# Kernel tuning notes

Hardware: AMD Instinct MI355X
Metric: run time of the kernel (lower is better)

Reference implementation:

```python
import jax, jax.numpy as jnp
import numpy as np

N_NODES = 50000


def gcn_conv(x, W, b, src, dst, n_nodes):
    """PyG GCNConv: h = x @ W; symmetric-normalized aggregation with self-loops; + bias."""
    h = x @ W  # [N, F_out]
    ones = jnp.ones(src.shape[0], dtype=h.dtype)
    # degree including the self-loop (edge weight 1)
    deg = jax.ops.segment_sum(ones, dst, num_segments=n_nodes) + 1.0
    dinv = jax.lax.rsqrt(deg)  # deg >= 1, always valid
    norm = dinv[src] * dinv[dst]  # [E]
    msgs = h[src] * norm[:, None]  # [E, F_out]
    agg = jax.ops.segment_sum(msgs, dst, num_segments=n_nodes)
    agg = agg + h * (dinv * dinv)[:, None]  # self-loop contribution, norm = dinv_i^2
    return agg + b


def setup_inputs() -> dict:
    key = jax.random.key(0)
    ks = jax.random.split(key, 8)
    n, f_in, f_hid, f_out, n_edges = N_NODES, 128, 128, 40, 800000
    x = jax.random.normal(ks[0], (n, f_in), dtype=jnp.float32)
    edge_index = jax.random.randint(ks[1], (2, n_edges), 0, n, dtype=jnp.int64)
    new_edge_indexs = jax.random.randint(ks[2], (2, 1000), 0, n, dtype=jnp.int64)
    # Glorot init like PyG defaults
    s1 = (6.0 / (f_in + f_hid)) ** 0.5
    s2 = (6.0 / (f_hid + f_out)) ** 0.5
    W1 = jax.random.uniform(ks[3], (f_in, f_hid), jnp.float32, -s1, s1)
    b1 = jnp.zeros((f_hid,), jnp.float32)
    W2 = jax.random.uniform(ks[4], (f_hid, f_out), jnp.float32, -s2, s2)
    b2 = jnp.zeros((f_out,), jnp.float32)
    return {"x": x, "W1": W1, "b1": b1, "W2": W2, "b2": b2,
            "edge_index": edge_index, "new_edge_indexs": new_edge_indexs}


def reference(x, W1, b1, W2, b2, edge_index, new_edge_indexs):
    src, dst = edge_index[0], edge_index[1]
    h = gcn_conv(x, W1, b1, src, dst, N_NODES)
    h = jax.nn.relu(h)
    # dropout(p=0.5) is identity in eval mode (training=False)
    h = gcn_conv(h, W2, b2, src, dst, N_NODES)
    return jax.nn.log_softmax(h, axis=-1)
```

## Files before the change

kernel.cpp:

```cpp
#include <hip/hip_runtime.h>
#include <hip/hip_bf16.h>

#define N_NODES 50000
#define N_EDGES 800000
#define F_IN    128
#define F_HID   128
#define F_OUT   40
#define N_TILES (N_NODES / 16)

#define NBIN      98
#define BIN_SHIFT 9
#define EPB       1024
#define CAP       32
#define GBIN_CAP  9216

#define CVT_BLOCKS ((F_IN * F_HID + 48 * F_HID) / 256)
#define DEGZ_BLOCKS 196
#define BIN_BLOCKS ((N_EDGES + EPB - 1) / EPB)
#define G1_BLOCKS  ((N_TILES + 3) / 4)

typedef __attribute__((ext_vector_type(8))) short bf16x8;
typedef __attribute__((ext_vector_type(4))) float f32x4;

__device__ __forceinline__ float2 unpack_bf2(unsigned u) {
    float2 r;
    r.x = __uint_as_float(u << 16);
    r.y = __uint_as_float(u & 0xffff0000u);
    return r;
}
__device__ __forceinline__ unsigned pack_bf2(float x, float y) {
    union { unsigned u; __hip_bfloat16 h[2]; } cv;
    cv.h[0] = __float2bfloat16(x);
    cv.h[1] = __float2bfloat16(y);
    return cv.u;
}
__device__ __forceinline__ short bfraw(float v) {
    __hip_bfloat16 h = __float2bfloat16(v);
    return *(short*)&h;
}
__device__ __forceinline__ float bf16u_to_f32(unsigned short us) {
    return __uint_as_float(((unsigned)us) << 16);
}

__device__ __forceinline__ int ld_src(const unsigned int* w, int is64, int e) {
    return is64 ? (int)w[2 * e] : (int)w[e];
}
__device__ __forceinline__ int ld_dst(const unsigned int* w, int is64, int e) {
    return is64 ? (int)w[2 * (N_EDGES + e)] : (int)w[N_EDGES + e];
}

__global__ void k_init(const unsigned int* __restrict__ ew,
                       const float* __restrict__ W1, const float* __restrict__ W2,
                       __hip_bfloat16* __restrict__ w1t, __hip_bfloat16* __restrict__ w2t,
                       int* __restrict__ flag, int* __restrict__ gcnt,
                       int* __restrict__ deg) {
    int b = blockIdx.x, t = threadIdx.x;
    if (b < CVT_BLOCKS) {
        int idx = b * 256 + t;
        if (idx < F_IN * F_HID) {
            int n = idx >> 7, k = idx & 127;
            w1t[idx] = __float2bfloat16(W1[k * F_HID + n]);
        } else {
            int j = idx - F_IN * F_HID;
            int n = j >> 7, k = j & 127;
            w2t[j] = __float2bfloat16(n < F_OUT ? W2[k * F_OUT + n] : 0.f);
        }
        return;
    }
    if (b < CVT_BLOCKS + DEGZ_BLOCKS) {
        int i = (b - CVT_BLOCKS) * 256 + t;
        if (i < N_NODES) deg[i] = 0;
        return;
    }
    __shared__ int nz;
    if (t == 0) nz = 0;
    __syncthreads();
    int local = 0;
    for (int i = t; i < 4096; i += 256)
        if (ew[2 * i + 1] != 0u) local = 1;
    if (local) atomicOr(&nz, 1);
    if (t < NBIN) gcnt[t] = 0;
    __syncthreads();
    if (t == 0) flag[0] = (nz == 0) ? 1 : 0;
}

__global__ void k_bindeg(const unsigned int* __restrict__ ew, const int* __restrict__ flag,
                         int* __restrict__ gcnt, unsigned* __restrict__ gbin,
                         int* __restrict__ deg) {
    __shared__ unsigned buf[NBIN][CAP];
    __shared__ int cnt[NBIN];
    __shared__ int base[NBIN];
    int t = threadIdx.x;
    for (int i = t; i < NBIN; i += 256) cnt[i] = 0;
    __syncthreads();
    int is64 = flag[0];
    int e0 = blockIdx.x * EPB;
    int n = min(EPB, N_EDGES - e0);
    for (int i = t; i < n; i += 256) {
        int e = e0 + i;
        int s = ld_src(ew, is64, e), d = ld_dst(ew, is64, e);
        atomicAdd(&deg[d], 1);
        unsigned rec = (unsigned)s | ((unsigned)d << 16);
        int b = d >> BIN_SHIFT;
        int c = atomicAdd(&cnt[b], 1);
        if (c < CAP) buf[b][c] = rec;
        else {
            int g = atomicAdd(&gcnt[b], 1);
            gbin[(size_t)b * GBIN_CAP + g] = rec;
        }
    }
    __syncthreads();
    if (t < NBIN) {
        int m = min(cnt[t], CAP);
        base[t] = atomicAdd(&gcnt[t], m);
        cnt[t] = m;
    }
    __syncthreads();
    int wave = t >> 6, lane = t & 63;
    for (int b = wave; b < NBIN; b += 4) {
        int m = cnt[b], bs = base[b];
        for (int i = lane; i < m; i += 64)
            gbin[(size_t)b * GBIN_CAP + bs + i] = buf[b][i];
    }
}

__global__ void k_scatg1(const int* __restrict__ gcnt, const unsigned* __restrict__ gbin,
                         const int* __restrict__ deg,
                         int* __restrict__ rowptr, unsigned* __restrict__ srcw,
                         const float* __restrict__ x, const __hip_bfloat16* __restrict__ w1t,
                         __hip_bfloat16* __restrict__ h1b) {
    __shared__ int pos[512];
    __shared__ int s2[256];
    __shared__ int gall[NBIN];
    __shared__ int bbase;
    int t = threadIdx.x;
    if (blockIdx.x < NBIN) {
        int b = blockIdx.x;
        if (t < NBIN) gall[t] = gcnt[t];
        int base512 = b << BIN_SHIFT;
        int i0 = base512 + 2 * t, i1 = i0 + 1;
        int d0 = (i0 < N_NODES) ? deg[i0] : 0;
        int d1 = (i1 < N_NODES) ? deg[i1] : 0;
        __syncthreads();
        if (t == 0) {
            int s = 0;
            for (int i = 0; i < b; i++) s += gall[i];
            bbase = s;
        }
        s2[t] = d0 + d1;
        __syncthreads();
        for (int off = 1; off < 256; off <<= 1) {
            int u = (t >= off) ? s2[t - off] : 0;
            __syncthreads();
            s2[t] += u;
            __syncthreads();
        }
        int ebase = bbase + s2[t] - d0 - d1;
        if (i0 < N_NODES) rowptr[i0] = ebase;
        if (i1 < N_NODES) rowptr[i1] = ebase + d0;
        pos[2 * t] = ebase;
        pos[2 * t + 1] = ebase + d0;
        if (b == 0 && t == 0) rowptr[N_NODES] = N_EDGES;
        __syncthreads();
        int n = gall[b];
        const unsigned* rec = gbin + (size_t)b * GBIN_CAP;
        for (int i = t; i < n; i += 256) {
            unsigned r = rec[i];
            int dl = (int)(r >> 16) - base512;
            int slot = atomicAdd(&pos[dl], 1);
            srcw[slot] = r & 0xFFFFu;
        }
        return;
    }
    int wave = t >> 6, lane = t & 63;
    int tile = (blockIdx.x - NBIN) * 4 + wave;
    if (tile >= N_TILES) return;
    int node0 = tile * 16;
    int m = lane & 15, q = lane >> 4;
    float dv[4];
#pragma unroll
    for (int r = 0; r < 4; r++)
        dv[r] = rsqrtf((float)deg[node0 + q * 4 + r] + 1.f);
    bf16x8 A[4];
    const float* arow = x + (size_t)(node0 + m) * F_IN + q * 8;
#pragma unroll
    for (int kt = 0; kt < 4; kt++) {
        float4 f0 = *(const float4*)(arow + kt * 32);
        float4 f1 = *(const float4*)(arow + kt * 32 + 4);
        bf16x8 a;
        a[0] = bfraw(f0.x); a[1] = bfraw(f0.y); a[2] = bfraw(f0.z); a[3] = bfraw(f0.w);
        a[4] = bfraw(f1.x); a[5] = bfraw(f1.y); a[6] = bfraw(f1.z); a[7] = bfraw(f1.w);
        A[kt] = a;
    }
#pragma unroll
    for (int c = 0; c < 8; c++) {
        f32x4 acc = {0.f, 0.f, 0.f, 0.f};
        const __hip_bfloat16* brow = w1t + (size_t)(c * 16 + m) * F_IN + q * 8;
#pragma unroll
        for (int kt = 0; kt < 4; kt++) {
            bf16x8 B = *(const bf16x8*)(brow + kt * 32);
            acc = __builtin_amdgcn_mfma_f32_16x16x32_bf16(A[kt], B, acc, 0, 0, 0);
        }
#pragma unroll
        for (int r = 0; r < 4; r++)
            h1b[(size_t)(node0 + q * 4 + r) * F_HID + c * 16 + m] =
                __float2bfloat16(acc[r] * dv[r]);
    }
}

__global__ void k_agg1g2(const int* __restrict__ rowptr, const unsigned* __restrict__ srcw,
                         const int* __restrict__ deg, const __hip_bfloat16* __restrict__ h1b,
                         const float* __restrict__ b1, const __hip_bfloat16* __restrict__ w2t,
                         __hip_bfloat16* __restrict__ h2b) {
    __shared__ __align__(16) short h1r[16][136];
    __shared__ float dvs[16];
    int t = threadIdx.x, wave = t >> 6, lane = t & 63;
    int node0 = blockIdx.x * 16;
    const unsigned* h1u = (const unsigned*)h1b;
#pragma unroll
    for (int i = 0; i < 4; i++) {
        int row = wave * 4 + i;
        int node = node0 + row;
        float di = rsqrtf((float)deg[node] + 1.f);
        int beg = __builtin_amdgcn_readfirstlane(rowptr[node]);
        int end = __builtin_amdgcn_readfirstlane(rowptr[node + 1]);
        float2 acc = unpack_bf2(h1u[(size_t)node * 64 + lane]);
        int e = beg;
        for (; e + 7 < end; e += 8) {
            unsigned p[8];
#pragma unroll
            for (int j = 0; j < 8; j++) p[j] = srcw[e + j];
            unsigned u[8];
#pragma unroll
            for (int j = 0; j < 8; j++)
                u[j] = h1u[(size_t)p[j] * 64 + lane];
#pragma unroll
            for (int j = 0; j < 8; j++) {
                float2 v = unpack_bf2(u[j]);
                acc.x += v.x;
                acc.y += v.y;
            }
        }
        for (; e < end; e++) {
            unsigned p = srcw[e];
            float2 v = unpack_bf2(h1u[(size_t)p * 64 + lane]);
            acc.x += v.x;
            acc.y += v.y;
        }
        float2 bb = ((const float2*)b1)[lane];
        acc.x = fmaxf(acc.x * di + bb.x, 0.f);
        acc.y = fmaxf(acc.y * di + bb.y, 0.f);
        ((unsigned*)&h1r[row][0])[lane] = pack_bf2(acc.x, acc.y);
        if (lane == 0) dvs[row] = di;
    }
    __syncthreads();
    if (wave < 3) {
        int m = lane & 15, q = lane >> 4;
        bf16x8 A[4];
#pragma unroll
        for (int kt = 0; kt < 4; kt++)
            A[kt] = *(const bf16x8*)(&h1r[m][q * 8 + kt * 32]);
        int c = wave;
        f32x4 acc = {0.f, 0.f, 0.f, 0.f};
        const __hip_bfloat16* brow = w2t + (size_t)(c * 16 + m) * F_HID + q * 8;
#pragma unroll
        for (int kt = 0; kt < 4; kt++) {
            bf16x8 B = *(const bf16x8*)(brow + kt * 32);
            acc = __builtin_amdgcn_mfma_f32_16x16x32_bf16(A[kt], B, acc, 0, 0, 0);
        }
        int col = c * 16 + m;
        if (col < F_OUT) {
#pragma unroll
            for (int r = 0; r < 4; r++)
                h2b[(size_t)(node0 + q * 4 + r) * F_OUT + col] =
                    __float2bfloat16(acc[r] * dvs[q * 4 + r]);
        }
    }
}

__global__ void k_agg2f(const int* __restrict__ rowptr, const unsigned* __restrict__ srcw,
                        const int* __restrict__ deg,
                        const unsigned short* __restrict__ h2b,
                        const float* __restrict__ b2, float* __restrict__ out) {
    int wave = threadIdx.x >> 6, lane = threadIdx.x & 63;
    int node = blockIdx.x * 4 + wave;
    float di = rsqrtf((float)deg[node] + 1.f);
    int beg = __builtin_amdgcn_readfirstlane(rowptr[node]);
    int end = __builtin_amdgcn_readfirstlane(rowptr[node + 1]);
    int l = (lane < F_OUT) ? lane : 0;
    float acc = bf16u_to_f32(h2b[(size_t)node * F_OUT + l]);
    int e = beg;
    for (; e + 7 < end; e += 8) {
        unsigned p[8];
#pragma unroll
        for (int j = 0; j < 8; j++) p[j] = srcw[e + j];
        float v[8];
#pragma unroll
        for (int j = 0; j < 8; j++)
            v[j] = bf16u_to_f32(h2b[(size_t)p[j] * F_OUT + l]);
#pragma unroll
        for (int j = 0; j < 8; j++)
            acc += v[j];
    }
    for (; e < end; e++) {
        unsigned p = srcw[e];
        acc += bf16u_to_f32(h2b[(size_t)p * F_OUT + l]);
    }
    float v = (lane < F_OUT) ? acc * di + b2[lane] : -INFINITY;
    float m = v;
    for (int off = 32; off; off >>= 1) m = fmaxf(m, __shfl_xor(m, off));
    float ex = (lane < F_OUT) ? __expf(v - m) : 0.f;
    float ssum = ex;
    for (int off = 32; off; off >>= 1) ssum += __shfl_xor(ssum, off);
    float ls = __logf(ssum);
    if (lane < F_OUT)
        out[(size_t)node * F_OUT + lane] = v - m - ls;
}

extern "C" void kernel_launch(void* const* d_in, const int* in_sizes, int n_in,
                              void* d_out, int out_size, void* d_ws, size_t ws_size,
                              hipStream_t stream) {
    const float* x  = (const float*)d_in[0];
    const float* W1 = (const float*)d_in[1];
    const float* b1 = (const float*)d_in[2];
    const float* W2 = (const float*)d_in[3];
    const float* b2 = (const float*)d_in[4];
    const unsigned int* ew = (const unsigned int*)d_in[5];
    float* out = (float*)d_out;

    char* ws = (char*)d_ws;
    int*   flag     = (int*)ws;   ws += 256;
    int*   gcnt     = (int*)ws;   ws += 512;
    int*   deg      = (int*)ws;   ws += ((N_NODES * 4 + 255) / 256) * 256;
    int*   rowptr   = (int*)ws;   ws += (((N_NODES + 1) * 4 + 255) / 256) * 256;
    unsigned* gbin  = (unsigned*)ws; ws += (size_t)NBIN * GBIN_CAP * 4;
    unsigned* srcw  = (unsigned*)ws; ws += (size_t)N_EDGES * 4;
    __hip_bfloat16* w1t  = (__hip_bfloat16*)ws; ws += F_IN * F_HID * 2;
    __hip_bfloat16* w2t  = (__hip_bfloat16*)ws; ws += 48 * F_HID * 2;
    __hip_bfloat16* h1b  = (__hip_bfloat16*)ws; ws += (size_t)N_NODES * F_HID * 2;
    __hip_bfloat16* h2b  = (__hip_bfloat16*)ws; ws += (size_t)N_NODES * F_OUT * 2;

    k_init   <<<CVT_BLOCKS + DEGZ_BLOCKS + 1, 256, 0, stream>>>(ew, W1, W2, w1t, w2t,
                                                                flag, gcnt, deg);
    k_bindeg <<<BIN_BLOCKS, 256, 0, stream>>>(ew, flag, gcnt, gbin, deg);
    k_scatg1 <<<NBIN + G1_BLOCKS, 256, 0, stream>>>(gcnt, gbin, deg, rowptr, srcw,
                                                    x, w1t, h1b);
    k_agg1g2 <<<N_NODES / 16, 256, 0, stream>>>(rowptr, srcw, deg, h1b, b1, w2t, h2b);
    k_agg2f  <<<N_NODES / 4, 256, 0, stream>>>(rowptr, srcw, deg,
                                               (const unsigned short*)h2b, b2, out);
}
```

Baseline: 219.9 us.

## Replace binned CSR build with global-atomic histogram, scan and scatter

Drops the shared-memory binning pass and per-bin staging buffer. Degrees are now counted with direct global atomics inside the init kernel, and each scan block computes its prefix from the deg array rather than from bin counts. A separate scatter kernel then places each edge's source via a global atomic on a per-node position array. This cuts one pass of staging traffic and the bin-capacity limits, but adds a kernel launch, two streams of random global atomics, and a per-block redundant prefix sum over deg. Edge order within a row now becomes nondeterministic.

```diff
diff --git a/kernel.cpp b/kernel.cpp
--- a/kernel.cpp
+++ b/kernel.cpp
@@ -10,14 +10,12 @@
 
 #define NBIN      98
 #define BIN_SHIFT 9
-#define EPB       1024
-#define CAP       32
-#define GBIN_CAP  9216
 
 #define CVT_BLOCKS ((F_IN * F_HID + 48 * F_HID) / 256)
-#define DEGZ_BLOCKS 196
-#define BIN_BLOCKS ((N_EDGES + EPB - 1) / EPB)
+#define HIST_BLOCKS 1564
+#define SC_BLOCKS   1564
 #define G1_BLOCKS  ((N_TILES + 3) / 4)
+#define ZERO_BLOCKS ((N_NODES + 255) / 256)
 
 typedef __attribute__((ext_vector_type(8))) short bf16x8;
 typedef __attribute__((ext_vector_type(4))) float f32x4;
@@ -49,11 +47,15 @@
     return is64 ? (int)w[2 * (N_EDGES + e)] : (int)w[N_EDGES + e];
 }
 
+__global__ void k_zero(int* __restrict__ deg) {
+    int i = blockIdx.x * 256 + threadIdx.x;
+    if (i < N_NODES) deg[i] = 0;
+}
+
 __global__ void k_init(const unsigned int* __restrict__ ew,
                        const float* __restrict__ W1, const float* __restrict__ W2,
                        __hip_bfloat16* __restrict__ w1t, __hip_bfloat16* __restrict__ w2t,
-                       int* __restrict__ flag, int* __restrict__ gcnt,
-                       int* __restrict__ deg) {
+                       int* __restrict__ flag, int* __restrict__ deg) {
     int b = blockIdx.x, t = threadIdx.x;
     if (b < CVT_BLOCKS) {
         int idx = b * 256 + t;
@@ -67,9 +69,24 @@
         }
         return;
     }
-    if (b < CVT_BLOCKS + DEGZ_BLOCKS) {
-        int i = (b - CVT_BLOCKS) * 256 + t;
-        if (i < N_NODES) deg[i] = 0;
+    if (b < CVT_BLOCKS + HIST_BLOCKS) {
+        __shared__ int nzs;
+        if (t == 0) nzs = 0;
+        __syncthreads();
+        int loc = 0;
+        for (int i = t; i < 2048; i += 256) loc |= (ew[2 * i + 1] != 0u);
+        if (loc) nzs = 1;
+        __syncthreads();
+        int is64 = (nzs == 0);
+        int e0 = (b - CVT_BLOCKS) * 512;
+#pragma unroll
+        for (int j = 0; j < 2; j++) {
+            int e = e0 + t + j * 256;
+            if (e < N_EDGES) {
+                int d = ld_dst(ew, is64, e);
+                atomicAdd(&deg[d], 1);
+            }
+        }
         return;
     }
     __shared__ int nz;
@@ -79,76 +96,33 @@
     for (int i = t; i < 4096; i += 256)
         if (ew[2 * i + 1] != 0u) local = 1;
     if (local) atomicOr(&nz, 1);
-    if (t < NBIN) gcnt[t] = 0;
     __syncthreads();
     if (t == 0) flag[0] = (nz == 0) ? 1 : 0;
 }
 
-__global__ void k_bindeg(const unsigned int* __restrict__ ew, const int* __restrict__ flag,
-                         int* __restrict__ gcnt, unsigned* __restrict__ gbin,
-                         int* __restrict__ deg) {
-    __shared__ unsigned buf[NBIN][CAP];
-    __shared__ int cnt[NBIN];
-    __shared__ int base[NBIN];
-    int t = threadIdx.x;
-    for (int i = t; i < NBIN; i += 256) cnt[i] = 0;
-    __syncthreads();
-    int is64 = flag[0];
-    int e0 = blockIdx.x * EPB;
-    int n = min(EPB, N_EDGES - e0);
-    for (int i = t; i < n; i += 256) {
-        int e = e0 + i;
-        int s = ld_src(ew, is64, e), d = ld_dst(ew, is64, e);
-        atomicAdd(&deg[d], 1);
-        unsigned rec = (unsigned)s | ((unsigned)d << 16);
-        int b = d >> BIN_SHIFT;
-        int c = atomicAdd(&cnt[b], 1);
-        if (c < CAP) buf[b][c] = rec;
-        else {
-            int g = atomicAdd(&gcnt[b], 1);
-            gbin[(size_t)b * GBIN_CAP + g] = rec;
-        }
-    }
-    __syncthreads();
-    if (t < NBIN) {
-        int m = min(cnt[t], CAP);
-        base[t] = atomicAdd(&gcnt[t], m);
-        cnt[t] = m;
-    }
-    __syncthreads();
-    int wave = t >> 6, lane = t & 63;
-    for (int b = wave; b < NBIN; b += 4) {
-        int m = cnt[b], bs = base[b];
-        for (int i = lane; i < m; i += 64)
-            gbin[(size_t)b * GBIN_CAP + bs + i] = buf[b][i];
-    }
-}
-
-__global__ void k_scatg1(const int* __restrict__ gcnt, const unsigned* __restrict__ gbin,
-                         const int* __restrict__ deg,
-                         int* __restrict__ rowptr, unsigned* __restrict__ srcw,
+__global__ void k_scang1(const int* __restrict__ deg,
+                         int* __restrict__ rowptr, int* __restrict__ pos,
                          const float* __restrict__ x, const __hip_bfloat16* __restrict__ w1t,
                          __hip_bfloat16* __restrict__ h1b) {
-    __shared__ int pos[512];
     __shared__ int s2[256];
-    __shared__ int gall[NBIN];
-    __shared__ int bbase;
+    __shared__ int wsum[4];
     int t = threadIdx.x;
     if (blockIdx.x < NBIN) {
         int b = blockIdx.x;
-        if (t < NBIN) gall[t] = gcnt[t];
         int base512 = b << BIN_SHIFT;
+        int acc = 0;
+        for (int j = t * 4; j < base512; j += 1024) {
+            int4 v = *(const int4*)(deg + j);
+            acc += v.x + v.y + v.z + v.w;
+        }
+        for (int off = 32; off; off >>= 1) acc += __shfl_down(acc, off);
+        if ((t & 63) == 0) wsum[t >> 6] = acc;
         int i0 = base512 + 2 * t, i1 = i0 + 1;
         int d0 = (i0 < N_NODES) ? deg[i0] : 0;
         int d1 = (i1 < N_NODES) ? deg[i1] : 0;
-        __syncthreads();
-        if (t == 0) {
-            int s = 0;
-            for (int i = 0; i < b; i++) s += gall[i];
-            bbase = s;
-        }
         s2[t] = d0 + d1;
         __syncthreads();
+        int bbase = wsum[0] + wsum[1] + wsum[2] + wsum[3];
         for (int off = 1; off < 256; off <<= 1) {
             int u = (t >= off) ? s2[t - off] : 0;
             __syncthreads();
@@ -156,20 +130,9 @@
             __syncthreads();
         }
         int ebase = bbase + s2[t] - d0 - d1;
-        if (i0 < N_NODES) rowptr[i0] = ebase;
-        if (i1 < N_NODES) rowptr[i1] = ebase + d0;
-        pos[2 * t] = ebase;
-        pos[2 * t + 1] = ebase + d0;
+        if (i0 < N_NODES) { rowptr[i0] = ebase;      pos[i0] = ebase; }
+        if (i1 < N_NODES) { rowptr[i1] = ebase + d0; pos[i1] = ebase + d0; }
         if (b == 0 && t == 0) rowptr[N_NODES] = N_EDGES;
-        __syncthreads();
-        int n = gall[b];
-        const unsigned* rec = gbin + (size_t)b * GBIN_CAP;
-        for (int i = t; i < n; i += 256) {
-            unsigned r = rec[i];
-            int dl = (int)(r >> 16) - base512;
-            int slot = atomicAdd(&pos[dl], 1);
-            srcw[slot] = r & 0xFFFFu;
-        }
         return;
     }
     int wave = t >> 6, lane = t & 63;
@@ -206,6 +169,23 @@
             h1b[(size_t)(node0 + q * 4 + r) * F_HID + c * 16 + m] =
                 __float2bfloat16(acc[r] * dv[r]);
     }
+}
+
+__global__ void k_scat(const unsigned int* __restrict__ ew, const int* __restrict__ flag,
+                       int* __restrict__ pos, unsigned* __restrict__ srcw) {
+    int t = threadIdx.x;
+    int is64 = flag[0];
+    int e0 = blockIdx.x * 512;
+    int ea = e0 + t, eb = e0 + t + 256;
+    int s0 = 0, d0 = 0, s1 = 0, d1 = 0;
+    bool va = ea < N_EDGES, vb = eb < N_EDGES;
+    if (va) { s0 = ld_src(ew, is64, ea); d0 = ld_dst(ew, is64, ea); }
+    if (vb) { s1 = ld_src(ew, is64, eb); d1 = ld_dst(ew, is64, eb); }
+    int sl0 = 0, sl1 = 0;
+    if (va) sl0 = atomicAdd(&pos[d0], 1);
+    if (vb) sl1 = atomicAdd(&pos[d1], 1);
+    if (va) srcw[sl0] = (unsigned)s0;
+    if (vb) srcw[sl1] = (unsigned)s1;
 }
 
 __global__ void k_agg1g2(const int* __restrict__ rowptr, const unsigned* __restrict__ srcw,
@@ -330,21 +310,20 @@
 
     char* ws = (char*)d_ws;
     int*   flag     = (int*)ws;   ws += 256;
-    int*   gcnt     = (int*)ws;   ws += 512;
     int*   deg      = (int*)ws;   ws += ((N_NODES * 4 + 255) / 256) * 256;
     int*   rowptr   = (int*)ws;   ws += (((N_NODES + 1) * 4 + 255) / 256) * 256;
-    unsigned* gbin  = (unsigned*)ws; ws += (size_t)NBIN * GBIN_CAP * 4;
+    int*   pos      = (int*)ws;   ws += ((N_NODES * 4 + 255) / 256) * 256;
     unsigned* srcw  = (unsigned*)ws; ws += (size_t)N_EDGES * 4;
     __hip_bfloat16* w1t  = (__hip_bfloat16*)ws; ws += F_IN * F_HID * 2;
     __hip_bfloat16* w2t  = (__hip_bfloat16*)ws; ws += 48 * F_HID * 2;
     __hip_bfloat16* h1b  = (__hip_bfloat16*)ws; ws += (size_t)N_NODES * F_HID * 2;
     __hip_bfloat16* h2b  = (__hip_bfloat16*)ws; ws += (size_t)N_NODES * F_OUT * 2;
 
-    k_init   <<<CVT_BLOCKS + DEGZ_BLOCKS + 1, 256, 0, stream>>>(ew, W1, W2, w1t, w2t,
-                                                                flag, gcnt, deg);
-    k_bindeg <<<BIN_BLOCKS, 256, 0, stream>>>(ew, flag, gcnt, gbin, deg);
-    k_scatg1 <<<NBIN + G1_BLOCKS, 256, 0, stream>>>(gcnt, gbin, deg, rowptr, srcw,
-                                                    x, w1t, h1b);
+    k_zero   <<<ZERO_BLOCKS, 256, 0, stream>>>(deg);
+    k_init   <<<CVT_BLOCKS + HIST_BLOCKS + 1, 256, 0, stream>>>(ew, W1, W2, w1t, w2t,
+                                                                flag, deg);
+    k_scang1 <<<NBIN + G1_BLOCKS, 256, 0, stream>>>(deg, rowptr, pos, x, w1t, h1b);
+    k_scat   <<<SC_BLOCKS, 256, 0, stream>>>(ew, flag, pos, srcw);
     k_agg1g2 <<<N_NODES / 16, 256, 0, stream>>>(rowptr, srcw, deg, h1b, b1, w2t, h2b);
     k_agg2f  <<<N_NODES / 4, 256, 0, stream>>>(rowptr, srcw, deg,
                                                (const unsigned short*)h2b, b2, out);
```

Result: slower. 243.4 us (+10.7%).
